# Optimization experiments

Hardware: AMD Instinct MI355X
Metric: run time of the kernel (lower is better)

The kernel has to match this reference:

```python
import jax, jax.numpy as jnp
import numpy as np

N = 64            # HiPPO order
DT = 1.0 / 512.0  # discretization timestep ~ 1/seq_len


def _hippo_legt_discrete(n, dt):
    """Continuous HiPPO-LegT (A,B) then bilinear (Tustin) discretization,
    matching scipy.signal.cont2discrete(..., method='bilinear')."""
    Q = np.arange(n, dtype=np.float64)
    R = (2 * Q + 1)[:, None]
    j, i = np.meshgrid(Q, Q)
    A = np.where(i < j, -1.0, (-1.0) ** (i - j + 1)) * R
    B = (-1.0) ** Q[:, None] * R  # (n, 1)
    I = np.eye(n)
    ima = I - (dt / 2.0) * A
    Ad = np.linalg.solve(ima, I + (dt / 2.0) * A)
    Bd = np.linalg.solve(ima, dt * B).squeeze(-1)  # (n,)
    return Ad, Bd


def setup_inputs() -> dict:
    key = jax.random.key(0)
    inputs = jax.random.normal(key, (16, 128, 512), dtype=jnp.float32)  # (b, d, L)
    Ad, Bd = _hippo_legt_discrete(N, DT)
    return {
        "inputs": inputs,
        "A": jnp.asarray(Ad, dtype=jnp.float32),  # (N, N)
        "B": jnp.asarray(Bd, dtype=jnp.float32),  # (N,)
    }


def reference(inputs, A, B):
    # inputs: (b, d, L) -> iterate over last axis, state c: (b, d, N)
    fs = jnp.moveaxis(inputs, -1, 0)  # (L, b, d)
    c0 = jnp.zeros(inputs.shape[:-1] + (A.shape[0],), dtype=inputs.dtype)

    def step(c, f):
        # c_t = c_{t-1} @ A^T + f_t[..., None] * B   (F.linear(c, A) == c @ A^T)
        c_new = c @ A.T + f[..., None] * B
        return c_new, c_new

    _, cs = jax.lax.scan(step, c0, fs)
    return cs  # (L, b, d, N)
```

## Files before the change

kernel.cpp:

```cpp
#include <hip/hip_runtime.h>


typedef _Float16 half8  __attribute__((ext_vector_type(8)));
typedef _Float16 half4t __attribute__((ext_vector_type(4)));
typedef float    f32x4  __attribute__((ext_vector_type(4)));

#define SEQN 2048
#define LT   512

__device__ __forceinline__ void mul64(const float* XT, const float* Y,
                                      float* outT, float* outN, int t) {
  const int r = (t >> 5) * 4;
  const int c = (t & 31) * 2;
  float a00 = 0.f, a01 = 0.f, a10 = 0.f, a11 = 0.f;
  float a20 = 0.f, a21 = 0.f, a30 = 0.f, a31 = 0.f;
#pragma unroll 4
  for (int l = 0; l < 64; ++l) {
    const float4 x = *(const float4*)(XT + l * 64 + r);
    const float2 y = *(const float2*)(Y + l * 64 + c);
    a00 += x.x * y.x; a01 += x.x * y.y;
    a10 += x.y * y.x; a11 += x.y * y.y;
    a20 += x.z * y.x; a21 += x.z * y.y;
    a30 += x.w * y.x; a31 += x.w * y.y;
  }
  __syncthreads();
  if (outT) {
    outT[(c + 0) * 64 + r + 0] = a00; outT[(c + 1) * 64 + r + 0] = a01;
    outT[(c + 0) * 64 + r + 1] = a10; outT[(c + 1) * 64 + r + 1] = a11;
    outT[(c + 0) * 64 + r + 2] = a20; outT[(c + 1) * 64 + r + 2] = a21;
    outT[(c + 0) * 64 + r + 3] = a30; outT[(c + 1) * 64 + r + 3] = a31;
  }
  if (outN) {
    outN[(r + 0) * 64 + c + 0] = a00; outN[(r + 0) * 64 + c + 1] = a01;
    outN[(r + 1) * 64 + c + 0] = a10; outN[(r + 1) * 64 + c + 1] = a11;
    outN[(r + 2) * 64 + c + 0] = a20; outN[(r + 2) * 64 + c + 1] = a21;
    outN[(r + 3) * 64 + c + 0] = a30; outN[(r + 3) * 64 + c + 1] = a31;
  }
  __syncthreads();
}

__global__ __launch_bounds__(512) void power_kernel(
    const float* __restrict__ A, const float* __restrict__ B,
    _Float16* __restrict__ Tg, float* __restrict__ Kg) {
  __shared__ float S[4096];
  __shared__ float STr[4096];
  __shared__ float RT[4096];
  const int t = threadIdx.x;
  const int d = blockIdx.x + 1;

  for (int i = t; i < 4096; i += 512) {
    const float v = A[i];
    S[i] = v;
    STr[(i & 63) * 64 + (i >> 6)] = v;
  }
  __syncthreads();

  bool rvalid = false;
  int e = d;
  while (e) {
    if (e & 1) {
      if (!rvalid) {
        for (int i = t; i < 4096; i += 512) RT[i] = STr[i];
        rvalid = true;
        __syncthreads();
      } else {
        mul64(RT, S, RT, nullptr, t);
      }
    }
    e >>= 1;
    if (e) mul64(STr, S, STr, S, t);
  }
  for (int i = t; i < 4096; i += 512) {
    const int n = i >> 6, m = i & 63;
    Tg[(size_t)((d - 1) * 64 + n) * 128 + m] = (_Float16)RT[m * 64 + n];
  }
  if (d < 64 && t < 64) {
    float s = 0.f;
    for (int m = 0; m < 64; ++m) s += RT[m * 64 + t] * B[m];
    Kg[d * 64 + t] = s;
  }
  if (d == 1 && t < 64) Kg[t] = B[t];
}

__global__ __launch_bounds__(256) void pack_kernel(
    const float* __restrict__ Kg, _Float16* __restrict__ Tg) {
  const int tau = blockIdx.x;
  const int t = threadIdx.x;
  const int n = t >> 2;
  const int j0 = (t & 3) * 16;
#pragma unroll
  for (int jj = 0; jj < 16; ++jj) {
    const int j = j0 + jj;
    const _Float16 v =
        (j <= tau) ? (_Float16)Kg[(tau - j) * 64 + n] : (_Float16)0.f;
    Tg[(size_t)(tau * 64 + n) * 128 + 64 + j] = v;
  }
}

__global__ __launch_bounds__(256) void chunk_gemm(
    const float* __restrict__ f, const _Float16* __restrict__ Tg,
    const float* __restrict__ carry, float* __restrict__ out, int chunk) {
  __shared__ _Float16 Xs[128 * 136];
  __shared__ _Float16 Ws[128 * 72];

  const int tid = threadIdx.x;
  const int bn = blockIdx.x;
  const int bm = blockIdx.y;
  const int lane = tid & 63, wid = tid >> 6;
  const int wm = wid >> 1, wn = wid & 1;
  const int l15 = lane & 15, quad = lane >> 4;

  {
    const int r = tid >> 1, h = tid & 1;
    const int seq = bm * 128 + r;
    if (h == 0) {
      if (carry) {
        const float4* s = (const float4*)(carry + (size_t)seq * 64);
#pragma unroll
        for (int i = 0; i < 16; ++i) {
          const float4 v = s[i];
          half4t hv = {(_Float16)v.x, (_Float16)v.y, (_Float16)v.z,
                       (_Float16)v.w};
          *(half4t*)&Xs[r * 136 + i * 4] = hv;
        }
      }
    } else {
      const float4* s = (const float4*)(f + (size_t)seq * LT + chunk * 64);
#pragma unroll
      for (int i = 0; i < 16; ++i) {
        const float4 v = s[i];
        half4t hv = {(_Float16)v.x, (_Float16)v.y, (_Float16)v.z,
                     (_Float16)v.w};
        *(half4t*)&Xs[r * 136 + 64 + i * 4] = hv;
      }
    }
  }

  f32x4 acc[4][4];
  const f32x4 z = {0.f, 0.f, 0.f, 0.f};
#pragma unroll
  for (int i = 0; i < 4; ++i)
#pragma unroll
    for (int j = 0; j < 4; ++j) acc[i][j] = z;

  const int kh0 = carry ? 0 : 1;
  for (int kh = kh0; kh < 2; ++kh) {
    if (kh != kh0) __syncthreads();
    {
      const int col = tid >> 1, h = tid & 1;
      const uint4* s = (const uint4*)(Tg + (size_t)(bn * 128 + col) * 128 +
                                      kh * 64 + h * 32);
#pragma unroll
      for (int i = 0; i < 4; ++i)
        *(uint4*)&Ws[col * 72 + h * 32 + i * 8] = s[i];
    }
    __syncthreads();

#pragma unroll
    for (int kk = 0; kk < 2; ++kk) {
      half8 av[4], bv[4];
#pragma unroll
      for (int fm = 0; fm < 4; ++fm)
        av[fm] = *(const half8*)&Xs[(wm * 64 + fm * 16 + l15) * 136 + kh * 64 +
                                    kk * 32 + quad * 8];
#pragma unroll
      for (int fn = 0; fn < 4; ++fn)
        bv[fn] = *(const half8*)&Ws[(wn * 64 + fn * 16 + l15) * 72 + kk * 32 +
                                    quad * 8];
#pragma unroll
      for (int fm = 0; fm < 4; ++fm)
#pragma unroll
        for (int fn = 0; fn < 4; ++fn)
          acc[fm][fn] = __builtin_amdgcn_mfma_f32_16x16x32_f16(
              av[fm], bv[fn], acc[fm][fn], 0, 0, 0);
    }
  }

  const int taug = chunk * 64 + bn * 2 + wn;
#pragma unroll
  for (int fm = 0; fm < 4; ++fm) {
#pragma unroll
    for (int r = 0; r < 4; ++r) {
      const size_t row =
          (size_t)taug * SEQN + (bm * 128 + wm * 64 + fm * 16 + quad * 4 + r);
      float* o = out + row * 64 + l15;
#pragma unroll
      for (int fn = 0; fn < 4; ++fn) o[fn * 16] = acc[fm][fn][r];
    }
  }
}

extern "C" void kernel_launch(void* const* d_in, const int* in_sizes, int n_in,
                              void* d_out, int out_size, void* d_ws,
                              size_t ws_size, hipStream_t stream) {
  const float* f = (const float*)d_in[0];
  const float* A = (const float*)d_in[1];
  const float* B = (const float*)d_in[2];
  float* out = (float*)d_out;

  _Float16* Tg = (_Float16*)d_ws;
  float* Kg = (float*)((char*)d_ws + 4096 * 128 * 2);

  power_kernel<<<64, 512, 0, stream>>>(A, B, Tg, Kg);
  pack_kernel<<<64, 256, 0, stream>>>(Kg, Tg);
  for (int k = 0; k < 8; ++k) {
    const float* carry =
        (k == 0) ? nullptr : out + (size_t)(64 * k - 1) * SEQN * 64;
    chunk_gemm<<<dim3(32, 16), 256, 0, stream>>>(f, Tg, carry, out, k);
  }
}
```

Before: 351.6 us.

## Precompute chunk boundary states with a scan kernel and launch all chunks at once

Adds a scan kernel that computes each sequence's state at every 64-step chunk boundary using A^64 and the impulse-response rows. This removes the serial dependency between chunk GEMM launches, so a single 3D-grid launch covers all 8 chunks and replaces the 8 back-to-back launches. The MFMA operands are also swapped so each lane writes contiguous float4 outputs. In exchange it adds a small sequential FP32 scan and a boundary buffer in the workspace.

```diff
diff --git a/kernel.cpp b/kernel.cpp
--- a/kernel.cpp
+++ b/kernel.cpp
@@ -41,7 +41,8 @@
 
 __global__ __launch_bounds__(512) void power_kernel(
     const float* __restrict__ A, const float* __restrict__ B,
-    _Float16* __restrict__ Tg, float* __restrict__ Kg) {
+    _Float16* __restrict__ Tg, float* __restrict__ Kg,
+    float* __restrict__ A64g) {
   __shared__ float S[4096];
   __shared__ float STr[4096];
   __shared__ float RT[4096];
@@ -80,6 +81,12 @@
     Kg[d * 64 + t] = s;
   }
   if (d == 1 && t < 64) Kg[t] = B[t];
+  if (d == 64) {
+    for (int i = t; i < 4096; i += 512) {
+      const int n = i >> 6, m = i & 63;
+      A64g[i] = RT[m * 64 + n];
+    }
+  }
 }
 
 __global__ __launch_bounds__(256) void pack_kernel(
@@ -97,42 +104,67 @@
   }
 }
 
+__global__ __launch_bounds__(256) void scan_kernel(
+    const float* __restrict__ f, const float* __restrict__ A64g,
+    const float* __restrict__ Kg, float* __restrict__ bound) {
+  __shared__ float A64s[64 * 65];
+  __shared__ float Kxs[64 * 65];
+  __shared__ float fs[4][64];
+  __shared__ float cs[4][64];
+  const int tid = threadIdx.x;
+  const int n = tid & 63, s = tid >> 6;
+  const int seq = blockIdx.x * 4 + s;
+
+  for (int i = tid; i < 4096; i += 256) {
+    const int r = i >> 6, c = i & 63;
+    A64s[r * 65 + c] = A64g[i];
+    Kxs[r * 65 + c] = Kg[(63 - c) * 64 + r];
+  }
+  cs[s][n] = 0.f;
+  bound[(size_t)seq * 64 + n] = 0.f;
+  __syncthreads();
+
+  for (int k = 0; k < 8; ++k) {
+    fs[s][n] = f[(size_t)seq * LT + k * 64 + n];
+    __syncthreads();
+    float u = 0.f, v = 0.f;
+#pragma unroll 8
+    for (int j = 0; j < 64; ++j) {
+      u += Kxs[n * 65 + j] * fs[s][j];
+      v += A64s[n * 65 + j] * cs[s][j];
+    }
+    __syncthreads();
+    const float cn = u + v;
+    cs[s][n] = cn;
+    if (k < 7) bound[((size_t)(k + 1) * SEQN + seq) * 64 + n] = cn;
+    __syncthreads();
+  }
+}
+
 __global__ __launch_bounds__(256) void chunk_gemm(
     const float* __restrict__ f, const _Float16* __restrict__ Tg,
-    const float* __restrict__ carry, float* __restrict__ out, int chunk) {
+    const float* __restrict__ bound, float* __restrict__ out) {
   __shared__ _Float16 Xs[128 * 136];
   __shared__ _Float16 Ws[128 * 72];
 
   const int tid = threadIdx.x;
-  const int bn = blockIdx.x;
-  const int bm = blockIdx.y;
+  const int bn = blockIdx.x, bm = blockIdx.y, chunk = blockIdx.z;
   const int lane = tid & 63, wid = tid >> 6;
   const int wm = wid >> 1, wn = wid & 1;
   const int l15 = lane & 15, quad = lane >> 4;
+  const float* carry = bound + (size_t)chunk * SEQN * 64;
 
   {
     const int r = tid >> 1, h = tid & 1;
     const int seq = bm * 128 + r;
-    if (h == 0) {
-      if (carry) {
-        const float4* s = (const float4*)(carry + (size_t)seq * 64);
-#pragma unroll
-        for (int i = 0; i < 16; ++i) {
-          const float4 v = s[i];
-          half4t hv = {(_Float16)v.x, (_Float16)v.y, (_Float16)v.z,
-                       (_Float16)v.w};
-          *(half4t*)&Xs[r * 136 + i * 4] = hv;
-        }
-      }
-    } else {
-      const float4* s = (const float4*)(f + (size_t)seq * LT + chunk * 64);
-#pragma unroll
-      for (int i = 0; i < 16; ++i) {
-        const float4 v = s[i];
-        half4t hv = {(_Float16)v.x, (_Float16)v.y, (_Float16)v.z,
-                     (_Float16)v.w};
-        *(half4t*)&Xs[r * 136 + 64 + i * 4] = hv;
-      }
+    const float4* s = h ? (const float4*)(f + (size_t)seq * LT + chunk * 64)
+                        : (const float4*)(carry + (size_t)seq * 64);
+    _Float16* dst = &Xs[r * 136 + h * 64];
+#pragma unroll
+    for (int i = 0; i < 16; ++i) {
+      const float4 v = s[i];
+      half4t hv = {(_Float16)v.x, (_Float16)v.y, (_Float16)v.z, (_Float16)v.w};
+      *(half4t*)(dst + i * 4) = hv;
     }
   }
 
@@ -143,9 +175,8 @@
 #pragma unroll
     for (int j = 0; j < 4; ++j) acc[i][j] = z;
 
-  const int kh0 = carry ? 0 : 1;
-  for (int kh = kh0; kh < 2; ++kh) {
-    if (kh != kh0) __syncthreads();
+  for (int kh = 0; kh < 2; ++kh) {
+    if (kh) __syncthreads();
     {
       const int col = tid >> 1, h = tid & 1;
       const uint4* s = (const uint4*)(Tg + (size_t)(bn * 128 + col) * 128 +
@@ -158,21 +189,21 @@
 
 #pragma unroll
     for (int kk = 0; kk < 2; ++kk) {
-      half8 av[4], bv[4];
+      half8 wv[4], xv[4];
 #pragma unroll
       for (int fm = 0; fm < 4; ++fm)
-        av[fm] = *(const half8*)&Xs[(wm * 64 + fm * 16 + l15) * 136 + kh * 64 +
+        wv[fm] = *(const half8*)&Ws[(wn * 64 + fm * 16 + l15) * 72 + kk * 32 +
+                                    quad * 8];
+#pragma unroll
+      for (int fn = 0; fn < 4; ++fn)
+        xv[fn] = *(const half8*)&Xs[(wm * 64 + fn * 16 + l15) * 136 + kh * 64 +
                                     kk * 32 + quad * 8];
-#pragma unroll
-      for (int fn = 0; fn < 4; ++fn)
-        bv[fn] = *(const half8*)&Ws[(wn * 64 + fn * 16 + l15) * 72 + kk * 32 +
-                                    quad * 8];
 #pragma unroll
       for (int fm = 0; fm < 4; ++fm)
 #pragma unroll
         for (int fn = 0; fn < 4; ++fn)
           acc[fm][fn] = __builtin_amdgcn_mfma_f32_16x16x32_f16(
-              av[fm], bv[fn], acc[fm][fn], 0, 0, 0);
+              wv[fm], xv[fn], acc[fm][fn], 0, 0, 0);
     }
   }
 
@@ -180,12 +211,10 @@
 #pragma unroll
   for (int fm = 0; fm < 4; ++fm) {
 #pragma unroll
-    for (int r = 0; r < 4; ++r) {
-      const size_t row =
-          (size_t)taug * SEQN + (bm * 128 + wm * 64 + fm * 16 + quad * 4 + r);
-      float* o = out + row * 64 + l15;
-#pragma unroll
-      for (int fn = 0; fn < 4; ++fn) o[fn * 16] = acc[fm][fn][r];
+    for (int fn = 0; fn < 4; ++fn) {
+      const int seq = bm * 128 + wm * 64 + fn * 16 + l15;
+      const int nb = fm * 16 + quad * 4;
+      *(f32x4*)(out + ((size_t)taug * SEQN + seq) * 64 + nb) = acc[fm][fn];
     }
   }
 }
@@ -198,14 +227,14 @@
   const float* B = (const float*)d_in[2];
   float* out = (float*)d_out;
 
-  _Float16* Tg = (_Float16*)d_ws;
-  float* Kg = (float*)((char*)d_ws + 4096 * 128 * 2);
-
-  power_kernel<<<64, 512, 0, stream>>>(A, B, Tg, Kg);
+  char* ws = (char*)d_ws;
+  _Float16* Tg = (_Float16*)ws;
+  float* Kg = (float*)(ws + (1 << 20));
+  float* A64g = (float*)(ws + (1 << 20) + (16 << 10));
+  float* bound = (float*)(ws + (1 << 20) + (32 << 10));
+
+  power_kernel<<<64, 512, 0, stream>>>(A, B, Tg, Kg, A64g);
   pack_kernel<<<64, 256, 0, stream>>>(Kg, Tg);
-  for (int k = 0; k < 8; ++k) {
-    const float* carry =
-        (k == 0) ? nullptr : out + (size_t)(64 * k - 1) * SEQN * 64;
-    chunk_gemm<<<dim3(32, 16), 256, 0, stream>>>(f, Tg, carry, out, k);
-  }
-}
+  scan_kernel<<<512, 256, 0, stream>>>(f, A64g, Kg, bound);
+  chunk_gemm<<<dim3(32, 16, 8), 256, 0, stream>>>(f, Tg, bound, out);
+}
```

New measurement: 358.2 us. Within noise of the previous version (+1.9%).
